# Optimization experiments

Hardware: AMD Instinct MI355X
Metric: run time of the kernel (lower is better)

The kernel has to match this reference:

```python
import jax, jax.numpy as jnp
import numpy as np

N_NODES = 100000
N_EDGES = 1600000
D = 64


def setup_inputs() -> dict:
    key = jax.random.key(0)
    k1, k2, k3, k4 = jax.random.split(key, 4)
    graph_embedding = jax.random.normal(k1, (N_NODES, D), dtype=jnp.float32)
    # xavier_uniform_ on a (1, D) tensor: bound = sqrt(6 / (1 + D))
    bound = float(np.sqrt(6.0 / (1 + D)))
    weight = jax.random.uniform(k2, (1, D), dtype=jnp.float32, minval=-bound, maxval=bound)
    src = jax.random.randint(k3, (N_EDGES,), 0, N_NODES, dtype=jnp.int32)
    dst = jax.random.randint(k4, (N_EDGES,), 0, N_NODES, dtype=jnp.int32)
    return {"graph_embedding": graph_embedding, "weight": weight, "src": src, "dst": dst}


def reference(graph_embedding, weight, src, dst):
    # emb = elu(x * w) per node, then copy_u/sum over edges:
    # out[d] = sum over edges (s -> d) of emb[s]
    emb = jax.nn.elu(graph_embedding * weight)          # [N, D]
    msgs = emb[src]                                     # [E, D] gathered source messages
    out = jax.ops.segment_sum(msgs, dst, num_segments=graph_embedding.shape[0])
    return out
```

## Files before the change

kernel.cpp:

```cpp
#include <hip/hip_runtime.h>

#define D 64
#define D4 (D / 4)
#define SBSHIFT 9
#define SBROWS 512
#define CHUNK_E 8192
#define STAGE_CAP 8704
#define NCH_MAX 256
#define NSB_MAX 256

typedef float f32x4 __attribute__((ext_vector_type(4)));

__device__ __forceinline__ float elu1(float z) {
    return z > 0.0f ? z : expm1f(z);
}

__device__ __forceinline__ unsigned int bfpair(float a, float b) {
    unsigned int ua = __float_as_uint(a);
    unsigned int ub = __float_as_uint(b);
    ua = (ua + 0x7FFFu + ((ua >> 16) & 1u)) >> 16;
    ub = (ub + 0x7FFFu + ((ub >> 16) & 1u)) & 0xFFFF0000u;
    return ub | ua;
}

__device__ __forceinline__ float bl16(int u) {
    return __uint_as_float((unsigned)u << 16);
}
__device__ __forceinline__ float bh16(int u) {
    return __uint_as_float((unsigned)u & 0xFFFF0000u);
}

__global__ void emb_kernel(const float* __restrict__ x,
                           const float* __restrict__ w,
                           uint4* __restrict__ emb16,
                           int total8) {
    int i = blockIdx.x * blockDim.x + threadIdx.x;
    if (i >= total8) return;
    f32x4 a = __builtin_nontemporal_load((const f32x4*)x + 2 * i);
    f32x4 b = __builtin_nontemporal_load((const f32x4*)x + 2 * i + 1);
    float4 wa = ((const float4*)w)[(2 * i) & 15];
    float4 wb = ((const float4*)w)[(2 * i + 1) & 15];
    uint4 o;
    o.x = bfpair(elu1(a.x * wa.x), elu1(a.y * wa.y));
    o.y = bfpair(elu1(a.z * wa.z), elu1(a.w * wa.w));
    o.z = bfpair(elu1(b.x * wb.x), elu1(b.y * wb.y));
    o.w = bfpair(elu1(b.z * wb.z), elu1(b.w * wb.w));
    emb16[i] = o;
}

__global__ __launch_bounds__(512) void chunk_sort_kernel(
        const int* __restrict__ src, const int* __restrict__ dst,
        int* __restrict__ slots_lin,
        int* __restrict__ cbase,
        int n_edges) {
    __shared__ int hist[256], base[256], cur[256];
    __shared__ int wsum[4];
    __shared__ int stage[CHUNK_E];
    const int tid = threadIdx.x;
    const int lane = tid & 63, wid = tid >> 6;
    const int c0  = blockIdx.x * CHUNK_E;
    const int kn  = min(CHUNK_E, n_edges - c0);
    const int kn4 = kn >> 2;
    const int tail = kn & 3;

    if (tid < 256) hist[tid] = 0;
    __syncthreads();
    const int4* dst4 = (const int4*)(dst + c0);
    for (int k = tid; k < kn4; k += 512) {
        int4 dv = dst4[k];
        atomicAdd(&hist[dv.x >> SBSHIFT], 1);
        atomicAdd(&hist[dv.y >> SBSHIFT], 1);
        atomicAdd(&hist[dv.z >> SBSHIFT], 1);
        atomicAdd(&hist[dv.w >> SBSHIFT], 1);
    }
    if (tid < tail)
        atomicAdd(&hist[dst[c0 + (kn4 << 2) + tid] >> SBSHIFT], 1);
    __syncthreads();
    int h = 0, incl = 0;
    if (tid < 256) {
        h = hist[tid];
        incl = h;
        #pragma unroll
        for (int off = 1; off < 64; off <<= 1) {
            int t = __shfl_up(incl, off, 64);
            if (lane >= off) incl += t;
        }
        if (lane == 63) wsum[wid] = incl;
    }
    __syncthreads();
    if (tid < 256) {
        int pre = 0;
        for (int k = 0; k < wid; k++) pre += wsum[k];
        int e = pre + incl - h;
        base[tid] = e;
        cur[tid]  = e;
    }
    __syncthreads();
    const int4* src4 = (const int4*)(src + c0);
    for (int k = tid; k < kn4; k += 512) {
        int4 dv = dst4[k];
        int4 sv = src4[k];
        int pos;
        pos = atomicAdd(&cur[dv.x >> SBSHIFT], 1);
        stage[pos] = ((dv.x & (SBROWS - 1)) << 17) | sv.x;
        pos = atomicAdd(&cur[dv.y >> SBSHIFT], 1);
        stage[pos] = ((dv.y & (SBROWS - 1)) << 17) | sv.y;
        pos = atomicAdd(&cur[dv.z >> SBSHIFT], 1);
        stage[pos] = ((dv.z & (SBROWS - 1)) << 17) | sv.z;
        pos = atomicAdd(&cur[dv.w >> SBSHIFT], 1);
        stage[pos] = ((dv.w & (SBROWS - 1)) << 17) | sv.w;
    }
    if (tid < tail) {
        int k = (kn4 << 2) + tid;
        int d = dst[c0 + k], s = src[c0 + k];
        int pos = atomicAdd(&cur[d >> SBSHIFT], 1);
        stage[pos] = ((d & (SBROWS - 1)) << 17) | s;
    }
    __syncthreads();
    for (int j = tid; j < kn; j += 512)
        slots_lin[c0 + j] = stage[j];
    if (tid < 256) cbase[blockIdx.x * 257 + tid] = base[tid];
    if (tid == 0)  cbase[blockIdx.x * 257 + 256] = kn;
}

__global__ void sbtot_kernel(const int* __restrict__ cbase,
                             int* __restrict__ sbtot, int NSB, int NCH) {
    __shared__ int wsum[4];
    const int s = blockIdx.x;
    const int tid = threadIdx.x;
    int v = 0;
    if (tid < NCH)
        v = cbase[tid * 257 + s + 1] - cbase[tid * 257 + s];
    #pragma unroll
    for (int off = 1; off < 64; off <<= 1) v += __shfl_xor(v, off, 64);
    if ((tid & 63) == 0) wsum[tid >> 6] = v;
    __syncthreads();
    if (tid == 0) sbtot[s] = wsum[0] + wsum[1] + wsum[2] + wsum[3];
}

__global__ void sb_scan2_kernel(const int* __restrict__ sbtot,
                                int* __restrict__ sb_base,
                                int* __restrict__ node_off,
                                int NSB, int n_nodes) {
    __shared__ int wsum[4];
    const int tid = threadIdx.x;
    int v = (tid < NSB) ? sbtot[tid] : 0;
    int incl = v;
    #pragma unroll
    for (int off = 1; off < 64; off <<= 1) {
        int t = __shfl_up(incl, off, 64);
        if ((tid & 63) >= off) incl += t;
    }
    if ((tid & 63) == 63) wsum[tid >> 6] = incl;
    __syncthreads();
    int pre = 0;
    for (int k = 0; k < (tid >> 6); k++) pre += wsum[k];
    if (tid < NSB) sb_base[tid] = pre + incl - v;
    if (tid == 0) {
        int g = wsum[0] + wsum[1] + wsum[2] + wsum[3];
        sb_base[NSB] = g;
        node_off[n_nodes] = g;
    }
}

__global__ __launch_bounds__(512) void fine_sort_kernel(
        const int* __restrict__ slots_lin,
        const int* __restrict__ cbase,
        const int* __restrict__ sb_base,
        int* __restrict__ sorted2,
        int* __restrict__ node_off,
        int n_nodes, int NCH) {
    __shared__ int rstart[NCH_MAX], rc[NCH_MAX];
    __shared__ int counts[SBROWS], cur[SBROWS];
    __shared__ int wsum[8];
    __shared__ int stage_out[STAGE_CAP];
    const int s = blockIdx.x;
    const int tid = threadIdx.x;
    const int wid = tid >> 6, lane = tid & 63;

    if (tid < NCH) {
        int a = cbase[tid * 257 + s];
        int b = cbase[tid * 257 + s + 1];
        rstart[tid] = tid * CHUNK_E + a;
        rc[tid] = b - a;
    }
    counts[tid] = 0;
    __syncthreads();
    const int sbb = sb_base[s];
    const int T   = sb_base[s + 1] - sbb;
    const bool fast = (T <= STAGE_CAP);
    for (int c = wid; c < NCH; c += 8) {
        int n = rc[c], st = rstart[c];
        for (int j = lane; j < n; j += 64)
            atomicAdd(&counts[((unsigned)slots_lin[st + j]) >> 17], 1);
    }
    __syncthreads();
    int v = counts[tid];
    int incl = v;
    #pragma unroll
    for (int off = 1; off < 64; off <<= 1) {
        int t = __shfl_up(incl, off, 64);
        if (lane >= off) incl += t;
    }
    if (lane == 63) wsum[wid] = incl;
    __syncthreads();
    int pre = 0;
    for (int k = 0; k < wid; k++) pre += wsum[k];
    int e0 = pre + incl - v;
    cur[tid] = fast ? e0 : sbb + e0;
    int g0 = (s << SBSHIFT) + tid;
    if (g0 < n_nodes) node_off[g0] = sbb + e0;
    __syncthreads();
    for (int c = wid; c < NCH; c += 8) {
        int n = rc[c], st = rstart[c];
        for (int j = lane; j < n; j += 64) {
            int pl = slots_lin[st + j];
            int r = ((unsigned)pl) >> 17;
            int pos = atomicAdd(&cur[r], 1);
            if (fast) stage_out[pos] = pl & 0x1FFFF;
            else      sorted2[pos]   = pl & 0x1FFFF;
        }
    }
    __syncthreads();
    if (fast) {
        for (int i = tid; i < T; i += 512)
            sorted2[sbb + i] = stage_out[i];
    }
}

__global__ void gather_sum_kernel(const unsigned int* __restrict__ emb16,
                                  const int* __restrict__ sorted2,
                                  const int* __restrict__ node_off,
                                  float* __restrict__ out, int n_nodes) {
    int wave = (blockIdx.x * blockDim.x + threadIdx.x) >> 6;
    if (wave >= n_nodes) return;
    const int lane = threadIdx.x & 63;
    const int g = lane >> 3;
    const int c = lane & 7;
    const int beg = node_off[wave], end = node_off[wave + 1];
    const int deg = end - beg;
    const int dmain = min(deg, 64);
    const int4* row = (const int4*)emb16;

    int myidx = 0;
    if (lane < dmain) myidx = __builtin_nontemporal_load(sorted2 + beg + lane);

    float acc[8] = {0.f, 0.f, 0.f, 0.f, 0.f, 0.f, 0.f, 0.f};

    for (int base = 0; base < dmain; base += 32) {
        const int m = dmain - base;
        int s0 = __shfl(myidx, base + g, 64);
        int s1 = __shfl(myidx, base + g + 8, 64);
        int s2 = __shfl(myidx, base + g + 16, 64);
        int s3 = __shfl(myidx, base + g + 24, 64);
        int4 u0 = make_int4(0, 0, 0, 0);
        int4 u1 = make_int4(0, 0, 0, 0);
        int4 u2 = make_int4(0, 0, 0, 0);
        int4 u3 = make_int4(0, 0, 0, 0);
        if (g < m)      u0 = row[s0 * 8 + c];
        if (g + 8 < m)  u1 = row[s1 * 8 + c];
        if (g + 16 < m) u2 = row[s2 * 8 + c];
        if (g + 24 < m) u3 = row[s3 * 8 + c];
        acc[0] += bl16(u0.x) + bl16(u1.x) + bl16(u2.x) + bl16(u3.x);
        acc[1] += bh16(u0.x) + bh16(u1.x) + bh16(u2.x) + bh16(u3.x);
        acc[2] += bl16(u0.y) + bl16(u1.y) + bl16(u2.y) + bl16(u3.y);
        acc[3] += bh16(u0.y) + bh16(u1.y) + bh16(u2.y) + bh16(u3.y);
        acc[4] += bl16(u0.z) + bl16(u1.z) + bl16(u2.z) + bl16(u3.z);
        acc[5] += bh16(u0.z) + bh16(u1.z) + bh16(u2.z) + bh16(u3.z);
        acc[6] += bl16(u0.w) + bl16(u1.w) + bl16(u2.w) + bl16(u3.w);
        acc[7] += bh16(u0.w) + bh16(u1.w) + bh16(u2.w) + bh16(u3.w);
    }
    for (int e = beg + 64 + g; e < end; e += 8) {
        int s0 = __builtin_nontemporal_load(sorted2 + e);
        int4 u0 = row[s0 * 8 + c];
        acc[0] += bl16(u0.x); acc[1] += bh16(u0.x);
        acc[2] += bl16(u0.y); acc[3] += bh16(u0.y);
        acc[4] += bl16(u0.z); acc[5] += bh16(u0.z);
        acc[6] += bl16(u0.w); acc[7] += bh16(u0.w);
    }
    #pragma unroll
    for (int off = 8; off <= 32; off <<= 1) {
        #pragma unroll
        for (int k = 0; k < 8; k++) acc[k] += __shfl_xor(acc[k], off, 64);
    }
    if (g == 0) {
        f32x4* out4 = (f32x4*)out;
        f32x4 o0 = {acc[0], acc[1], acc[2], acc[3]};
        f32x4 o1 = {acc[4], acc[5], acc[6], acc[7]};
        __builtin_nontemporal_store(o0, out4 + wave * D4 + c * 2);
        __builtin_nontemporal_store(o1, out4 + wave * D4 + c * 2 + 1);
    }
}

__global__ void zero_out_kernel(float* __restrict__ out, int total4) {
    int i = blockIdx.x * blockDim.x + threadIdx.x;
    if (i < total4) ((float4*)out)[i] = make_float4(0.f, 0.f, 0.f, 0.f);
}

__global__ void scatter_fused_kernel(const float* __restrict__ x,
                                     const float* __restrict__ w,
                                     const int* __restrict__ src,
                                     const int* __restrict__ dst,
                                     float* __restrict__ out, int n_edges) {
    int t = blockIdx.x * blockDim.x + threadIdx.x;
    int e = t >> 4;
    int c = t & 15;
    if (e >= n_edges) return;
    int s = src[e];
    int d = dst[e];
    float4 xv = ((const float4*)x)[s * D4 + c];
    float4 wv = ((const float4*)w)[c];
    float* o = out + d * D + c * 4;
    unsafeAtomicAdd(o + 0, elu1(xv.x * wv.x));
    unsafeAtomicAdd(o + 1, elu1(xv.y * wv.y));
    unsafeAtomicAdd(o + 2, elu1(xv.z * wv.z));
    unsafeAtomicAdd(o + 3, elu1(xv.w * wv.w));
}

extern "C" void kernel_launch(void* const* d_in, const int* in_sizes, int n_in,
                              void* d_out, int out_size, void* d_ws, size_t ws_size,
                              hipStream_t stream) {
    const float* x   = (const float*)d_in[0];
    const float* w   = (const float*)d_in[1];
    const int*   src = (const int*)d_in[2];
    const int*   dst = (const int*)d_in[3];
    float* out = (float*)d_out;

    const int n_nodes = in_sizes[0] / D;
    const int n_edges = in_sizes[2];
    const int total4  = n_nodes * D4;
    const int total8  = n_nodes * 8;
    const int block = 256;

    const int NSB = (n_nodes + SBROWS - 1) >> SBSHIFT;
    const int NCH = (n_edges + CHUNK_E - 1) / CHUNK_E;

    auto align16 = [](size_t v) { return (v + 15) & ~size_t(15); };
    const size_t emb_b      = align16((size_t)n_nodes * D * 2);
    const size_t slots_b    = align16((size_t)NCH * CHUNK_E * 4);
    const size_t cbase_b    = align16((size_t)NCH * 257 * 4);
    const size_t sbtot_b    = align16((size_t)NSB * 4);
    const size_t sbbase_b   = align16((size_t)(NSB + 1) * 4);
    const size_t sorted2_b  = align16((size_t)n_edges * 4);
    const size_t nodeoff_b  = align16((size_t)(n_nodes + 1) * 4);
    const size_t need = emb_b + slots_b + cbase_b + sbtot_b + sbbase_b +
                        sorted2_b + nodeoff_b;

    if (ws_size >= need && n_nodes <= 131072 && NSB <= NSB_MAX && NCH <= NCH_MAX) {
        char* p = (char*)d_ws;
        unsigned int* emb16 = (unsigned int*)p;  p += emb_b;
        int* slots_lin = (int*)p;  p += slots_b;
        int* cbase     = (int*)p;  p += cbase_b;
        int* sbtot     = (int*)p;  p += sbtot_b;
        int* sb_base   = (int*)p;  p += sbbase_b;
        int* sorted2   = (int*)p;  p += sorted2_b;
        int* node_off  = (int*)p;

        emb_kernel<<<(total8 + block - 1) / block, block, 0, stream>>>(
            x, w, (uint4*)emb16, total8);
        chunk_sort_kernel<<<NCH, 512, 0, stream>>>(
            src, dst, slots_lin, cbase, n_edges);
        sbtot_kernel<<<NSB, 256, 0, stream>>>(cbase, sbtot, NSB, NCH);
        sb_scan2_kernel<<<1, 256, 0, stream>>>(sbtot, sb_base, node_off,
                                               NSB, n_nodes);
        fine_sort_kernel<<<NSB, 512, 0, stream>>>(
            slots_lin, cbase, sb_base, sorted2, node_off, n_nodes, NCH);
        const int wave_blocks = (n_nodes * 64 + block - 1) / block;
        gather_sum_kernel<<<wave_blocks, block, 0, stream>>>(
            emb16, sorted2, node_off, out, n_nodes);
    } else {
        zero_out_kernel<<<(total4 + block - 1) / block, block, 0, stream>>>(out, total4);
        const int nt = n_edges * 16;
        scatter_fused_kernel<<<(nt + block - 1) / block, block, 0, stream>>>(
            x, w, src, dst, out, n_edges);
    }
}
```

Measured before the change: 155.9 us.

## Replace two-level LDS bucket sort with global atomic counting sort for CSR build

Replaces the chunked superblock bucket sort (chunk sort, per-superblock totals, scan, fine sort in LDS) with a plain counting sort: a global atomic degree histogram, a two-pass block scan for node offsets, and an atomic scatter of source indices into CSR order. Degree zeroing is folded into the embedding kernel. This cuts kernel count, intermediate buffers and size limits, but relies on global atomics over 1.6M edges and produces non-coalesced scattered writes instead of LDS-staged ones. Edge order within a node becomes nondeterministic.

```diff
diff --git a/kernel.cpp b/kernel.cpp
--- a/kernel.cpp
+++ b/kernel.cpp
@@ -2,12 +2,6 @@
 
 #define D 64
 #define D4 (D / 4)
-#define SBSHIFT 9
-#define SBROWS 512
-#define CHUNK_E 8192
-#define STAGE_CAP 8704
-#define NCH_MAX 256
-#define NSB_MAX 256
 
 typedef float f32x4 __attribute__((ext_vector_type(4)));
 
@@ -33,8 +27,10 @@
 __global__ void emb_kernel(const float* __restrict__ x,
                            const float* __restrict__ w,
                            uint4* __restrict__ emb16,
-                           int total8) {
-    int i = blockIdx.x * blockDim.x + threadIdx.x;
+                           int* __restrict__ node_deg,
+                           int total8, int n_nodes) {
+    int i = blockIdx.x * blockDim.x + threadIdx.x;
+    if (i < n_nodes) node_deg[i] = 0;
     if (i >= total8) return;
     f32x4 a = __builtin_nontemporal_load((const f32x4*)x + 2 * i);
     f32x4 b = __builtin_nontemporal_load((const f32x4*)x + 2 * i + 1);
@@ -48,154 +44,29 @@
     emb16[i] = o;
 }
 
-__global__ __launch_bounds__(512) void chunk_sort_kernel(
-        const int* __restrict__ src, const int* __restrict__ dst,
-        int* __restrict__ slots_lin,
-        int* __restrict__ cbase,
-        int n_edges) {
-    __shared__ int hist[256], base[256], cur[256];
-    __shared__ int wsum[4];
-    __shared__ int stage[CHUNK_E];
-    const int tid = threadIdx.x;
-    const int lane = tid & 63, wid = tid >> 6;
-    const int c0  = blockIdx.x * CHUNK_E;
-    const int kn  = min(CHUNK_E, n_edges - c0);
-    const int kn4 = kn >> 2;
-    const int tail = kn & 3;
-
-    if (tid < 256) hist[tid] = 0;
-    __syncthreads();
-    const int4* dst4 = (const int4*)(dst + c0);
-    for (int k = tid; k < kn4; k += 512) {
-        int4 dv = dst4[k];
-        atomicAdd(&hist[dv.x >> SBSHIFT], 1);
-        atomicAdd(&hist[dv.y >> SBSHIFT], 1);
-        atomicAdd(&hist[dv.z >> SBSHIFT], 1);
-        atomicAdd(&hist[dv.w >> SBSHIFT], 1);
-    }
-    if (tid < tail)
-        atomicAdd(&hist[dst[c0 + (kn4 << 2) + tid] >> SBSHIFT], 1);
-    __syncthreads();
-    int h = 0, incl = 0;
-    if (tid < 256) {
-        h = hist[tid];
-        incl = h;
-        #pragma unroll
-        for (int off = 1; off < 64; off <<= 1) {
-            int t = __shfl_up(incl, off, 64);
-            if (lane >= off) incl += t;
-        }
-        if (lane == 63) wsum[wid] = incl;
-    }
-    __syncthreads();
-    if (tid < 256) {
-        int pre = 0;
-        for (int k = 0; k < wid; k++) pre += wsum[k];
-        int e = pre + incl - h;
-        base[tid] = e;
-        cur[tid]  = e;
-    }
-    __syncthreads();
-    const int4* src4 = (const int4*)(src + c0);
-    for (int k = tid; k < kn4; k += 512) {
-        int4 dv = dst4[k];
-        int4 sv = src4[k];
-        int pos;
-        pos = atomicAdd(&cur[dv.x >> SBSHIFT], 1);
-        stage[pos] = ((dv.x & (SBROWS - 1)) << 17) | sv.x;
-        pos = atomicAdd(&cur[dv.y >> SBSHIFT], 1);
-        stage[pos] = ((dv.y & (SBROWS - 1)) << 17) | sv.y;
-        pos = atomicAdd(&cur[dv.z >> SBSHIFT], 1);
-        stage[pos] = ((dv.z & (SBROWS - 1)) << 17) | sv.z;
-        pos = atomicAdd(&cur[dv.w >> SBSHIFT], 1);
-        stage[pos] = ((dv.w & (SBROWS - 1)) << 17) | sv.w;
-    }
-    if (tid < tail) {
-        int k = (kn4 << 2) + tid;
-        int d = dst[c0 + k], s = src[c0 + k];
-        int pos = atomicAdd(&cur[d >> SBSHIFT], 1);
-        stage[pos] = ((d & (SBROWS - 1)) << 17) | s;
-    }
-    __syncthreads();
-    for (int j = tid; j < kn; j += 512)
-        slots_lin[c0 + j] = stage[j];
-    if (tid < 256) cbase[blockIdx.x * 257 + tid] = base[tid];
-    if (tid == 0)  cbase[blockIdx.x * 257 + 256] = kn;
-}
-
-__global__ void sbtot_kernel(const int* __restrict__ cbase,
-                             int* __restrict__ sbtot, int NSB, int NCH) {
-    __shared__ int wsum[4];
-    const int s = blockIdx.x;
-    const int tid = threadIdx.x;
-    int v = 0;
-    if (tid < NCH)
-        v = cbase[tid * 257 + s + 1] - cbase[tid * 257 + s];
-    #pragma unroll
-    for (int off = 1; off < 64; off <<= 1) v += __shfl_xor(v, off, 64);
-    if ((tid & 63) == 0) wsum[tid >> 6] = v;
-    __syncthreads();
-    if (tid == 0) sbtot[s] = wsum[0] + wsum[1] + wsum[2] + wsum[3];
-}
-
-__global__ void sb_scan2_kernel(const int* __restrict__ sbtot,
-                                int* __restrict__ sb_base,
-                                int* __restrict__ node_off,
-                                int NSB, int n_nodes) {
-    __shared__ int wsum[4];
-    const int tid = threadIdx.x;
-    int v = (tid < NSB) ? sbtot[tid] : 0;
-    int incl = v;
-    #pragma unroll
-    for (int off = 1; off < 64; off <<= 1) {
-        int t = __shfl_up(incl, off, 64);
-        if ((tid & 63) >= off) incl += t;
-    }
-    if ((tid & 63) == 63) wsum[tid >> 6] = incl;
-    __syncthreads();
-    int pre = 0;
-    for (int k = 0; k < (tid >> 6); k++) pre += wsum[k];
-    if (tid < NSB) sb_base[tid] = pre + incl - v;
-    if (tid == 0) {
-        int g = wsum[0] + wsum[1] + wsum[2] + wsum[3];
-        sb_base[NSB] = g;
-        node_off[n_nodes] = g;
-    }
-}
-
-__global__ __launch_bounds__(512) void fine_sort_kernel(
-        const int* __restrict__ slots_lin,
-        const int* __restrict__ cbase,
-        const int* __restrict__ sb_base,
-        int* __restrict__ sorted2,
+__global__ void hist_kernel(const int* __restrict__ dst,
+                            int* __restrict__ node_deg, int n_edges) {
+    int i = blockIdx.x * blockDim.x + threadIdx.x;
+    const int n4 = n_edges >> 2;
+    if (i < n4) {
+        int4 dv = ((const int4*)dst)[i];
+        atomicAdd(&node_deg[dv.x], 1);
+        atomicAdd(&node_deg[dv.y], 1);
+        atomicAdd(&node_deg[dv.z], 1);
+        atomicAdd(&node_deg[dv.w], 1);
+    }
+    if (i < (n_edges & 3))
+        atomicAdd(&node_deg[dst[(n4 << 2) + i]], 1);
+}
+
+__global__ __launch_bounds__(512) void scan_block_kernel(
+        const int* __restrict__ node_deg,
         int* __restrict__ node_off,
-        int n_nodes, int NCH) {
-    __shared__ int rstart[NCH_MAX], rc[NCH_MAX];
-    __shared__ int counts[SBROWS], cur[SBROWS];
+        int* __restrict__ bsum, int n_nodes) {
     __shared__ int wsum[8];
-    __shared__ int stage_out[STAGE_CAP];
-    const int s = blockIdx.x;
-    const int tid = threadIdx.x;
-    const int wid = tid >> 6, lane = tid & 63;
-
-    if (tid < NCH) {
-        int a = cbase[tid * 257 + s];
-        int b = cbase[tid * 257 + s + 1];
-        rstart[tid] = tid * CHUNK_E + a;
-        rc[tid] = b - a;
-    }
-    counts[tid] = 0;
-    __syncthreads();
-    const int sbb = sb_base[s];
-    const int T   = sb_base[s + 1] - sbb;
-    const bool fast = (T <= STAGE_CAP);
-    for (int c = wid; c < NCH; c += 8) {
-        int n = rc[c], st = rstart[c];
-        for (int j = lane; j < n; j += 64)
-            atomicAdd(&counts[((unsigned)slots_lin[st + j]) >> 17], 1);
-    }
-    __syncthreads();
-    int v = counts[tid];
+    const int tid = threadIdx.x, lane = tid & 63, wid = tid >> 6;
+    const int g = blockIdx.x * 512 + tid;
+    int v = (g < n_nodes) ? node_deg[g] : 0;
     int incl = v;
     #pragma unroll
     for (int off = 1; off < 64; off <<= 1) {
@@ -206,25 +77,54 @@
     __syncthreads();
     int pre = 0;
     for (int k = 0; k < wid; k++) pre += wsum[k];
-    int e0 = pre + incl - v;
-    cur[tid] = fast ? e0 : sbb + e0;
-    int g0 = (s << SBSHIFT) + tid;
-    if (g0 < n_nodes) node_off[g0] = sbb + e0;
+    if (g < n_nodes) node_off[g] = pre + incl - v;
+    if (tid == 511) bsum[blockIdx.x] = pre + incl;
+}
+
+__global__ __launch_bounds__(512) void scan_add_kernel(
+        const int* __restrict__ bsum,
+        int* __restrict__ node_off,
+        int* __restrict__ cur, int n_nodes, int NBLK) {
+    __shared__ int sbase;
+    const int b = blockIdx.x, tid = threadIdx.x;
+    if (tid < 64) {
+        int p = 0;
+        for (int k = tid; k < b; k += 64) p += bsum[k];
+        #pragma unroll
+        for (int off = 1; off < 64; off <<= 1) p += __shfl_xor(p, off, 64);
+        if (tid == 0) sbase = p;
+    }
     __syncthreads();
-    for (int c = wid; c < NCH; c += 8) {
-        int n = rc[c], st = rstart[c];
-        for (int j = lane; j < n; j += 64) {
-            int pl = slots_lin[st + j];
-            int r = ((unsigned)pl) >> 17;
-            int pos = atomicAdd(&cur[r], 1);
-            if (fast) stage_out[pos] = pl & 0x1FFFF;
-            else      sorted2[pos]   = pl & 0x1FFFF;
-        }
-    }
-    __syncthreads();
-    if (fast) {
-        for (int i = tid; i < T; i += 512)
-            sorted2[sbb + i] = stage_out[i];
+    const int base = sbase;
+    const int g = b * 512 + tid;
+    if (g < n_nodes) {
+        int t = node_off[g] + base;
+        node_off[g] = t;
+        cur[g] = t;
+    }
+    if (b == NBLK - 1 && tid == 0)
+        node_off[n_nodes] = base + bsum[b];
+}
+
+__global__ void scatter_sort_kernel(const int* __restrict__ src,
+                                    const int* __restrict__ dst,
+                                    int* __restrict__ cur,
+                                    int* __restrict__ sorted2, int n_edges) {
+    int i = blockIdx.x * blockDim.x + threadIdx.x;
+    const int n4 = n_edges >> 2;
+    if (i < n4) {
+        int4 dv = ((const int4*)dst)[i];
+        int4 sv = ((const int4*)src)[i];
+        int p;
+        p = atomicAdd(&cur[dv.x], 1); sorted2[p] = sv.x;
+        p = atomicAdd(&cur[dv.y], 1); sorted2[p] = sv.y;
+        p = atomicAdd(&cur[dv.z], 1); sorted2[p] = sv.z;
+        p = atomicAdd(&cur[dv.w], 1); sorted2[p] = sv.w;
+    }
+    if (i < (n_edges & 3)) {
+        int k = (n4 << 2) + i;
+        int p = atomicAdd(&cur[dst[k]], 1);
+        sorted2[p] = src[k];
     }
 }
 
@@ -332,39 +232,36 @@
     const int total8  = n_nodes * 8;
     const int block = 256;
 
-    const int NSB = (n_nodes + SBROWS - 1) >> SBSHIFT;
-    const int NCH = (n_edges + CHUNK_E - 1) / CHUNK_E;
+    const int NBLK = (n_nodes + 511) >> 9;
 
     auto align16 = [](size_t v) { return (v + 15) & ~size_t(15); };
     const size_t emb_b      = align16((size_t)n_nodes * D * 2);
-    const size_t slots_b    = align16((size_t)NCH * CHUNK_E * 4);
-    const size_t cbase_b    = align16((size_t)NCH * 257 * 4);
-    const size_t sbtot_b    = align16((size_t)NSB * 4);
-    const size_t sbbase_b   = align16((size_t)(NSB + 1) * 4);
     const size_t sorted2_b  = align16((size_t)n_edges * 4);
     const size_t nodeoff_b  = align16((size_t)(n_nodes + 1) * 4);
-    const size_t need = emb_b + slots_b + cbase_b + sbtot_b + sbbase_b +
-                        sorted2_b + nodeoff_b;
-
-    if (ws_size >= need && n_nodes <= 131072 && NSB <= NSB_MAX && NCH <= NCH_MAX) {
+    const size_t deg_b      = align16((size_t)n_nodes * 4);
+    const size_t cur_b      = align16((size_t)n_nodes * 4);
+    const size_t bsum_b     = align16((size_t)NBLK * 4);
+    const size_t need = emb_b + sorted2_b + nodeoff_b + deg_b + cur_b + bsum_b;
+
+    if (ws_size >= need) {
         char* p = (char*)d_ws;
         unsigned int* emb16 = (unsigned int*)p;  p += emb_b;
-        int* slots_lin = (int*)p;  p += slots_b;
-        int* cbase     = (int*)p;  p += cbase_b;
-        int* sbtot     = (int*)p;  p += sbtot_b;
-        int* sb_base   = (int*)p;  p += sbbase_b;
-        int* sorted2   = (int*)p;  p += sorted2_b;
-        int* node_off  = (int*)p;
+        int* sorted2  = (int*)p;  p += sorted2_b;
+        int* node_off = (int*)p;  p += nodeoff_b;
+        int* node_deg = (int*)p;  p += deg_b;
+        int* cur      = (int*)p;  p += cur_b;
+        int* bsum     = (int*)p;
 
         emb_kernel<<<(total8 + block - 1) / block, block, 0, stream>>>(
-            x, w, (uint4*)emb16, total8);
-        chunk_sort_kernel<<<NCH, 512, 0, stream>>>(
-            src, dst, slots_lin, cbase, n_edges);
-        sbtot_kernel<<<NSB, 256, 0, stream>>>(cbase, sbtot, NSB, NCH);
-        sb_scan2_kernel<<<1, 256, 0, stream>>>(sbtot, sb_base, node_off,
-                                               NSB, n_nodes);
-        fine_sort_kernel<<<NSB, 512, 0, stream>>>(
-            slots_lin, cbase, sb_base, sorted2, node_off, n_nodes, NCH);
+            x, w, (uint4*)emb16, node_deg, total8, n_nodes);
+        const int e4blk = ((n_edges >> 2) + block) / block + 1;
+        hist_kernel<<<e4blk, block, 0, stream>>>(dst, node_deg, n_edges);
+        scan_block_kernel<<<NBLK, 512, 0, stream>>>(
+            node_deg, node_off, bsum, n_nodes);
+        scan_add_kernel<<<NBLK, 512, 0, stream>>>(
+            bsum, node_off, cur, n_nodes, NBLK);
+        scatter_sort_kernel<<<e4blk, block, 0, stream>>>(
+            src, dst, cur, sorted2, n_edges);
         const int wave_blocks = (n_nodes * 64 + block - 1) / block;
         gather_sum_kernel<<<wave_blocks, block, 0, stream>>>(
             emb16, sorted2, node_off, out, n_nodes);
```

New measurement: 322.0 us. 107% more time.

## Fuse embedding into chunk sort and compute superblock offsets inside fine sort

Applied to the files above, without the earlier changes.

The bf16 ELU embedding pass is folded into the chunk-sort kernel as a grid-stride loop, so it no longer needs its own launch. The separate superblock-total and scan kernels are removed. Each fine-sort block now derives its own base offset and edge count by reducing the per-chunk bases from cbase with wave shuffles. Fine sort also assigns 16 lanes per chunk segment instead of a full wave, since each segment holds only a few dozen edges. Together these cut three kernel launches and better fill the lanes, at the cost of some redundant reduction work in every block and extra register pressure in the fused kernel.

```diff
diff --git a/kernel.cpp b/kernel.cpp
--- a/kernel.cpp
+++ b/kernel.cpp
@@ -30,40 +30,38 @@
     return __uint_as_float((unsigned)u & 0xFFFF0000u);
 }
 
-__global__ void emb_kernel(const float* __restrict__ x,
-                           const float* __restrict__ w,
-                           uint4* __restrict__ emb16,
-                           int total8) {
-    int i = blockIdx.x * blockDim.x + threadIdx.x;
-    if (i >= total8) return;
-    f32x4 a = __builtin_nontemporal_load((const f32x4*)x + 2 * i);
-    f32x4 b = __builtin_nontemporal_load((const f32x4*)x + 2 * i + 1);
-    float4 wa = ((const float4*)w)[(2 * i) & 15];
-    float4 wb = ((const float4*)w)[(2 * i + 1) & 15];
-    uint4 o;
-    o.x = bfpair(elu1(a.x * wa.x), elu1(a.y * wa.y));
-    o.y = bfpair(elu1(a.z * wa.z), elu1(a.w * wa.w));
-    o.z = bfpair(elu1(b.x * wb.x), elu1(b.y * wb.y));
-    o.w = bfpair(elu1(b.z * wb.z), elu1(b.w * wb.w));
-    emb16[i] = o;
-}
-
-__global__ __launch_bounds__(512) void chunk_sort_kernel(
+__global__ __launch_bounds__(512) void chunk_emb_kernel(
+        const float* __restrict__ x, const float* __restrict__ w,
+        uint4* __restrict__ emb16,
         const int* __restrict__ src, const int* __restrict__ dst,
         int* __restrict__ slots_lin,
         int* __restrict__ cbase,
-        int n_edges) {
+        int total8, int n_edges) {
     __shared__ int hist[256], base[256], cur[256];
     __shared__ int wsum[4];
     __shared__ int stage[CHUNK_E];
     const int tid = threadIdx.x;
     const int lane = tid & 63, wid = tid >> 6;
+
+    if (tid < 256) hist[tid] = 0;
+    const int gsz = gridDim.x * 512;
+    for (int i = blockIdx.x * 512 + tid; i < total8; i += gsz) {
+        f32x4 a = __builtin_nontemporal_load((const f32x4*)x + 2 * i);
+        f32x4 b = __builtin_nontemporal_load((const f32x4*)x + 2 * i + 1);
+        float4 wa = ((const float4*)w)[(2 * i) & 15];
+        float4 wb = ((const float4*)w)[(2 * i + 1) & 15];
+        uint4 o;
+        o.x = bfpair(elu1(a.x * wa.x), elu1(a.y * wa.y));
+        o.y = bfpair(elu1(a.z * wa.z), elu1(a.w * wa.w));
+        o.z = bfpair(elu1(b.x * wb.x), elu1(b.y * wb.y));
+        o.w = bfpair(elu1(b.z * wb.z), elu1(b.w * wb.w));
+        emb16[i] = o;
+    }
+
     const int c0  = blockIdx.x * CHUNK_E;
     const int kn  = min(CHUNK_E, n_edges - c0);
     const int kn4 = kn >> 2;
     const int tail = kn & 3;
-
-    if (tid < 256) hist[tid] = 0;
     __syncthreads();
     const int4* dst4 = (const int4*)(dst + c0);
     for (int k = tid; k < kn4; k += 512) {
@@ -123,75 +121,45 @@
     if (tid == 0)  cbase[blockIdx.x * 257 + 256] = kn;
 }
 
-__global__ void sbtot_kernel(const int* __restrict__ cbase,
-                             int* __restrict__ sbtot, int NSB, int NCH) {
-    __shared__ int wsum[4];
-    const int s = blockIdx.x;
-    const int tid = threadIdx.x;
-    int v = 0;
-    if (tid < NCH)
-        v = cbase[tid * 257 + s + 1] - cbase[tid * 257 + s];
-    #pragma unroll
-    for (int off = 1; off < 64; off <<= 1) v += __shfl_xor(v, off, 64);
-    if ((tid & 63) == 0) wsum[tid >> 6] = v;
-    __syncthreads();
-    if (tid == 0) sbtot[s] = wsum[0] + wsum[1] + wsum[2] + wsum[3];
-}
-
-__global__ void sb_scan2_kernel(const int* __restrict__ sbtot,
-                                int* __restrict__ sb_base,
-                                int* __restrict__ node_off,
-                                int NSB, int n_nodes) {
-    __shared__ int wsum[4];
-    const int tid = threadIdx.x;
-    int v = (tid < NSB) ? sbtot[tid] : 0;
-    int incl = v;
-    #pragma unroll
-    for (int off = 1; off < 64; off <<= 1) {
-        int t = __shfl_up(incl, off, 64);
-        if ((tid & 63) >= off) incl += t;
-    }
-    if ((tid & 63) == 63) wsum[tid >> 6] = incl;
-    __syncthreads();
-    int pre = 0;
-    for (int k = 0; k < (tid >> 6); k++) pre += wsum[k];
-    if (tid < NSB) sb_base[tid] = pre + incl - v;
-    if (tid == 0) {
-        int g = wsum[0] + wsum[1] + wsum[2] + wsum[3];
-        sb_base[NSB] = g;
-        node_off[n_nodes] = g;
-    }
-}
-
 __global__ __launch_bounds__(512) void fine_sort_kernel(
         const int* __restrict__ slots_lin,
         const int* __restrict__ cbase,
-        const int* __restrict__ sb_base,
         int* __restrict__ sorted2,
         int* __restrict__ node_off,
         int n_nodes, int NCH) {
     __shared__ int rstart[NCH_MAX], rc[NCH_MAX];
     __shared__ int counts[SBROWS], cur[SBROWS];
-    __shared__ int wsum[8];
+    __shared__ int wsum[8], swa[8], swt[8];
     __shared__ int stage_out[STAGE_CAP];
     const int s = blockIdx.x;
     const int tid = threadIdx.x;
     const int wid = tid >> 6, lane = tid & 63;
-
+    const int sg = tid >> 4, l16 = tid & 15;
+
+    int va = 0, vt = 0;
     if (tid < NCH) {
         int a = cbase[tid * 257 + s];
         int b = cbase[tid * 257 + s + 1];
         rstart[tid] = tid * CHUNK_E + a;
         rc[tid] = b - a;
-    }
+        va = a;
+        vt = b - a;
+    }
+    #pragma unroll
+    for (int off = 1; off < 64; off <<= 1) {
+        va += __shfl_xor(va, off, 64);
+        vt += __shfl_xor(vt, off, 64);
+    }
+    if (lane == 0) { swa[wid] = va; swt[wid] = vt; }
     counts[tid] = 0;
     __syncthreads();
-    const int sbb = sb_base[s];
-    const int T   = sb_base[s + 1] - sbb;
+    int sbb = 0, T = 0;
+    #pragma unroll
+    for (int k = 0; k < 8; k++) { sbb += swa[k]; T += swt[k]; }
     const bool fast = (T <= STAGE_CAP);
-    for (int c = wid; c < NCH; c += 8) {
+    for (int c = sg; c < NCH; c += 32) {
         int n = rc[c], st = rstart[c];
-        for (int j = lane; j < n; j += 64)
+        for (int j = l16; j < n; j += 16)
             atomicAdd(&counts[((unsigned)slots_lin[st + j]) >> 17], 1);
     }
     __syncthreads();
@@ -210,10 +178,11 @@
     cur[tid] = fast ? e0 : sbb + e0;
     int g0 = (s << SBSHIFT) + tid;
     if (g0 < n_nodes) node_off[g0] = sbb + e0;
-    __syncthreads();
-    for (int c = wid; c < NCH; c += 8) {
+    if (s == gridDim.x - 1 && tid == 0) node_off[n_nodes] = sbb + T;
+    __syncthreads();
+    for (int c = sg; c < NCH; c += 32) {
         int n = rc[c], st = rstart[c];
-        for (int j = lane; j < n; j += 64) {
+        for (int j = l16; j < n; j += 16) {
             int pl = slots_lin[st + j];
             int r = ((unsigned)pl) >> 17;
             int pos = atomicAdd(&cur[r], 1);
@@ -339,32 +308,22 @@
     const size_t emb_b      = align16((size_t)n_nodes * D * 2);
     const size_t slots_b    = align16((size_t)NCH * CHUNK_E * 4);
     const size_t cbase_b    = align16((size_t)NCH * 257 * 4);
-    const size_t sbtot_b    = align16((size_t)NSB * 4);
-    const size_t sbbase_b   = align16((size_t)(NSB + 1) * 4);
     const size_t sorted2_b  = align16((size_t)n_edges * 4);
     const size_t nodeoff_b  = align16((size_t)(n_nodes + 1) * 4);
-    const size_t need = emb_b + slots_b + cbase_b + sbtot_b + sbbase_b +
-                        sorted2_b + nodeoff_b;
+    const size_t need = emb_b + slots_b + cbase_b + sorted2_b + nodeoff_b;
 
     if (ws_size >= need && n_nodes <= 131072 && NSB <= NSB_MAX && NCH <= NCH_MAX) {
         char* p = (char*)d_ws;
         unsigned int* emb16 = (unsigned int*)p;  p += emb_b;
         int* slots_lin = (int*)p;  p += slots_b;
         int* cbase     = (int*)p;  p += cbase_b;
-        int* sbtot     = (int*)p;  p += sbtot_b;
-        int* sb_base   = (int*)p;  p += sbbase_b;
         int* sorted2   = (int*)p;  p += sorted2_b;
         int* node_off  = (int*)p;
 
-        emb_kernel<<<(total8 + block - 1) / block, block, 0, stream>>>(
-            x, w, (uint4*)emb16, total8);
-        chunk_sort_kernel<<<NCH, 512, 0, stream>>>(
-            src, dst, slots_lin, cbase, n_edges);
-        sbtot_kernel<<<NSB, 256, 0, stream>>>(cbase, sbtot, NSB, NCH);
-        sb_scan2_kernel<<<1, 256, 0, stream>>>(sbtot, sb_base, node_off,
-                                               NSB, n_nodes);
+        chunk_emb_kernel<<<NCH, 512, 0, stream>>>(
+            x, w, (uint4*)emb16, src, dst, slots_lin, cbase, total8, n_edges);
         fine_sort_kernel<<<NSB, 512, 0, stream>>>(
-            slots_lin, cbase, sb_base, sorted2, node_off, n_nodes, NCH);
+            slots_lin, cbase, sorted2, node_off, n_nodes, NCH);
         const int wave_blocks = (n_nodes * 64 + block - 1) / block;
         gather_sum_kernel<<<wave_blocks, block, 0, stream>>>(
             emb16, sorted2, node_off, out, n_nodes);
```

New measurement: 149.7 us. -3.9%, faster.
